# Optimization experiments

Measured on AMD Instinct MI355X. Metric: run time of the kernel, lower is better.

Reference implementation:

```python
import jax, jax.numpy as jnp
import numpy as np

B, S, D = 2, 2048, 1024
H, DH = 16, 64
DM = 4096
NEG = 1e10


def setup_inputs() -> dict:
    key = jax.random.key(0)
    ks = jax.random.split(key, 8)
    sc = 1.0 / np.sqrt(D)
    return {
        "x": jax.random.normal(ks[0], (B, S, D), jnp.float32),
        "W_Q": jax.random.normal(ks[1], (H, DH, D), jnp.float32) * sc,
        "W_K": jax.random.normal(ks[2], (H, DH, D), jnp.float32) * sc,
        "W_V": jax.random.normal(ks[3], (H, DH, D), jnp.float32) * sc,
        "W_O": jax.random.normal(ks[4], (D, H * DH), jnp.float32) * sc,
        "W_in": jax.random.normal(ks[5], (DM, D), jnp.float32) * sc,
        "b_in": jnp.zeros((DM,), jnp.float32),
        "W_out": jax.random.normal(ks[6], (D, DM), jnp.float32) * sc,
        "b_out": jnp.zeros((D,), jnp.float32),
    }


def reference(x, W_Q, W_K, W_V, W_O, W_in, b_in, W_out, b_out):
    b, s, d = x.shape
    d_head = W_Q.shape[1]
    # --- Attention (faithful to original einsum/mask formulation) ---
    q = jnp.einsum('ihd,bpd->biph', W_Q, x)
    k = jnp.einsum('ihd,bpd->biph', W_K, x)
    v = jnp.einsum('ihd,bpd->biph', W_V, x)
    scores = jnp.einsum('biph,biqh->biqp', k, q)  # [b,i,q,p]
    # original: t.tril(scores) - 1e10 * (1 - triu(ones)) ; mask buffer is triu
    triu = jnp.triu(jnp.ones((s, s), x.dtype))
    masked = jnp.tril(scores) - NEG * (1.0 - triu)
    attn = jax.nn.softmax(masked / np.sqrt(d_head), axis=-1)
    z = jnp.einsum('biph,biqp->biqh', v, attn)          # [b,i,q,h]
    z_flat = z.transpose(0, 2, 1, 3).reshape(b, s, -1)   # b q (i h)
    attn_out = jnp.einsum('df,bqf->bqd', W_O, z_flat)
    # --- Block residual structure (as written: x = attn(x); x = x + x) ---
    mid = attn_out + attn_out
    # --- MLP ---
    pre = jnp.einsum('md,bpd->bpm', W_in, mid) + b_in
    h = jax.nn.relu(pre)
    mlp_out = jnp.einsum('dm,bpm->bpd', W_out, h) + b_out
    return mid + mlp_out
```

## Files before the change

kernel.cpp:

```cpp
#include <hip/hip_runtime.h>
#include <hip/hip_bf16.h>
#include <stdint.h>

typedef unsigned short ushort_t;
typedef __attribute__((ext_vector_type(8))) short short8;
typedef __attribute__((ext_vector_type(4))) float floatx4;

#define DEV __device__ __forceinline__

DEV ushort_t f2b(float f) {
  uint32_t x = __float_as_uint(f);
  uint32_t r = (x + 0x7FFFu + ((x >> 16) & 1u)) >> 16;
  return (ushort_t)r;
}
DEV float b2f(ushort_t u) { return __uint_as_float(((uint32_t)u) << 16); }

DEV void async16(const ushort_t* g, ushort_t* l) {
  __builtin_amdgcn_global_load_lds(
      (const __attribute__((address_space(1))) void*)g,
      (__attribute__((address_space(3))) void*)l, 16, 0, 0);
}

struct Cvt7 {
  const float* src[7];
  ushort_t* dst[7];
  unsigned start[8];
};
__global__ void cvt_all(Cvt7 a) {
  unsigned idx = blockIdx.x * blockDim.x + threadIdx.x;
  if (idx >= a.start[7]) return;
  int seg = 0;
#pragma unroll
  for (int j = 1; j < 7; j++) seg += (idx >= a.start[j]) ? 1 : 0;
  unsigned off = idx - a.start[seg];
  float4 v = ((const float4*)a.src[seg])[off];
  ((ushort4*)a.dst[seg])[off] = make_ushort4(f2b(v.x), f2b(v.y), f2b(v.z), f2b(v.w));
}

template <int MODE, int MT>
__launch_bounds__(256)
__global__ void gemm_bt(const ushort_t* __restrict__ A, const ushort_t* __restrict__ Bm,
                        int M, int N, int K,
                        ushort_t* __restrict__ outB, float* __restrict__ outF,
                        const float* __restrict__ bias) {
  constexpr int TM = 32 * MT;
  __shared__ alignas(16) ushort_t As[TM * 64];
  __shared__ alignas(16) ushort_t Bs[128 * 64];
  const int tid = threadIdx.x;
  const int wave = tid >> 6, lane = tid & 63;
  const int wm = wave >> 1, wn = wave & 1;
  const int m0 = blockIdx.y * TM, n0 = blockIdx.x * 128;

  floatx4 acc[MT][4];
#pragma unroll
  for (int i = 0; i < MT; i++)
#pragma unroll
    for (int j = 0; j < 4; j++) acc[i][j] = (floatx4){0.f, 0.f, 0.f, 0.f};

  const int r8 = lane >> 3;
  const int scol = (((lane & 7) ^ (r8 & 7)) * 8);
  const ushort_t* gA = A + (size_t)(m0 + wave * (TM / 4) + r8) * K + scol;
  const ushort_t* gB = Bm + (size_t)(n0 + wave * 32 + r8) * K + scol;
  ushort_t* lA = As + wave * (TM / 4) * 64;
  ushort_t* lB = Bs + wave * 2048;

  const int fr = lane & 15, fq = lane >> 4;
  const int sw = fr & 7;
  const ushort_t* rdA = As + (wm * 16 * MT + fr) * 64;
  const ushort_t* rdB = Bs + (wn * 64 + fr) * 64;

  for (int k0 = 0; k0 < K; k0 += 64) {
#pragma unroll
    for (int j = 0; j < MT; j++) async16(gA + (size_t)j * 8 * K, lA + j * 512);
#pragma unroll
    for (int j = 0; j < 4; j++) async16(gB + (size_t)j * 8 * K, lB + j * 512);
    gA += 64; gB += 64;
    __syncthreads();
#pragma unroll
    for (int h = 0; h < 2; h++) {
      const int co = ((h * 4 + fq) ^ sw) * 8;
      short8 af[MT], bfv[4];
#pragma unroll
      for (int mt = 0; mt < MT; mt++) af[mt] = *(const short8*)(rdA + mt * 16 * 64 + co);
#pragma unroll
      for (int nt = 0; nt < 4; nt++) bfv[nt] = *(const short8*)(rdB + nt * 16 * 64 + co);
#pragma unroll
      for (int mt = 0; mt < MT; mt++)
#pragma unroll
        for (int nt = 0; nt < 4; nt++)
          acc[mt][nt] = __builtin_amdgcn_mfma_f32_16x16x32_bf16(af[mt], bfv[nt], acc[mt][nt], 0, 0, 0);
    }
    __syncthreads();
  }

  const int crow = m0 + wm * 16 * MT + (lane >> 4) * 4;
  const int ccol = n0 + wn * 64 + (lane & 15);
#pragma unroll
  for (int mt = 0; mt < MT; mt++)
#pragma unroll
    for (int nt = 0; nt < 4; nt++) {
      floatx4 a = acc[mt][nt];
#pragma unroll
      for (int r = 0; r < 4; r++) {
        const int gm = crow + mt * 16 + r;
        const int gn = ccol + nt * 16;
        const size_t idx = (size_t)gm * N + gn;
        float v = a[r];
        if constexpr (MODE == 0) {
          outB[idx] = f2b(v);
        } else if constexpr (MODE == 1) {
          float t = 2.f * v;
          outB[idx] = f2b(t);
          outF[idx] = t + bias[gn];
        } else if constexpr (MODE == 2) {
          float t = v + bias[gn];
          outB[idx] = f2b(t > 0.f ? t : 0.f);
        } else {
          outF[idx] += v;
        }
      }
    }
}

__launch_bounds__(256)
__global__ void attn1(const ushort_t* __restrict__ qkv,
                      float* __restrict__ eG, float* __restrict__ psumG) {
  const int c = blockIdx.x & 31;
  const int i = (blockIdx.x >> 5) & 15;
  const int b = blockIdx.x >> 9;
  const int t = threadIdx.x, wave = t >> 6, h = t & 63;
  const size_t rowbase = (size_t)b * 2048 * 3072;
  float vacc = 0.f;
#pragma unroll 4
  for (int r = 0; r < 16; r++) {
    const int s = c * 64 + wave * 16 + r;
    const size_t rb = rowbase + (size_t)s * 3072 + i * 64 + h;
    float q = b2f(qkv[rb]);
    float k = b2f(qkv[rb + 1024]);
    float v = b2f(qkv[rb + 2048]);
    float d = q * k;
#pragma unroll
    for (int off = 32; off > 0; off >>= 1) d += __shfl_xor(d, off, 64);
    if (h == 0) eG[((size_t)(b * 16 + i)) * 2048 + s] = __expf(d * 0.125f);
    vacc += v;
  }
  __shared__ float vs[4][64];
  vs[wave][h] = vacc;
  __syncthreads();
  if (t < 64)
    psumG[(((size_t)(b * 16 + i)) * 32 + c) * 64 + t] =
        vs[0][t] + vs[1][t] + vs[2][t] + vs[3][t];
}

__launch_bounds__(256)
__global__ void attn2(const ushort_t* __restrict__ qkv,
                      const float* __restrict__ eG, const float* __restrict__ psumG,
                      ushort_t* __restrict__ Z) {
  const int wave = threadIdx.x >> 6, h = threadIdx.x & 63;
  const int c = (blockIdx.x & 7) * 4 + wave;
  const int i = (blockIdx.x >> 3) & 15;
  const int b = blockIdx.x >> 7;
  const size_t rowbase = (size_t)b * 2048 * 3072;
  const size_t pbase = ((size_t)(b * 16 + i)) * 32;
  float run = 0.f;
#pragma unroll 8
  for (int cc = c + 1; cc < 32; cc++) run += psumG[(pbase + cc) * 64 + h];
  const size_t ebase = ((size_t)(b * 16 + i)) * 2048;
  for (int t4 = 3; t4 >= 0; t4--) {
    float vv[16], ee[16];
#pragma unroll
    for (int j = 0; j < 16; j++) {
      const int s = c * 64 + t4 * 16 + j;
      vv[j] = b2f(qkv[rowbase + (size_t)s * 3072 + 2048 + i * 64 + h]);
      ee[j] = eG[ebase + s];
    }
#pragma unroll
    for (int j = 15; j >= 0; j--) {
      const int s = c * 64 + t4 * 16 + j;
      float z = (ee[j] * vv[j] + run) / (ee[j] + (float)(2047 - s));
      Z[((size_t)b * 2048 + s) * 1024 + i * 64 + h] = f2b(z);
      run += vv[j];
    }
  }
}

extern "C" void kernel_launch(void* const* d_in, const int* in_sizes, int n_in,
                              void* d_out, int out_size, void* d_ws, size_t ws_size,
                              hipStream_t stream) {
  const float* x     = (const float*)d_in[0];
  const float* W_Q   = (const float*)d_in[1];
  const float* W_K   = (const float*)d_in[2];
  const float* W_V   = (const float*)d_in[3];
  const float* W_O   = (const float*)d_in[4];
  const float* W_in  = (const float*)d_in[5];
  const float* b_in  = (const float*)d_in[6];
  const float* W_out = (const float*)d_in[7];
  const float* b_out = (const float*)d_in[8];
  float* out = (float*)d_out;

  char* base = (char*)d_ws;
  const size_t MB = 1048576;
  ushort_t* Xb    = (ushort_t*)(base + 0 * MB);
  ushort_t* Wqkv  = (ushort_t*)(base + 8 * MB);
  ushort_t* WOb   = (ushort_t*)(base + 14 * MB);
  ushort_t* Z     = (ushort_t*)(base + 16 * MB);
  ushort_t* QKV   = (ushort_t*)(base + 24 * MB);
  ushort_t* midb  = (ushort_t*)(base + 48 * MB);
  ushort_t* Winb  = (ushort_t*)(base + 56 * MB);
  ushort_t* Woutb = (ushort_t*)(base + 64 * MB);
  ushort_t* Hb    = (ushort_t*)(base + 72 * MB);
  float*    eG    = (float*)(base + 104 * MB);
  float*    psumG = (float*)(base + 104 * MB + 262144);

  Cvt7 ca;
  ca.src[0] = x;     ca.dst[0] = Xb;
  ca.src[1] = W_Q;   ca.dst[1] = Wqkv;
  ca.src[2] = W_K;   ca.dst[2] = Wqkv + 1048576;
  ca.src[3] = W_V;   ca.dst[3] = Wqkv + 2097152;
  ca.src[4] = W_O;   ca.dst[4] = WOb;
  ca.src[5] = W_in;  ca.dst[5] = Winb;
  ca.src[6] = W_out; ca.dst[6] = Woutb;
  unsigned n4s[7] = {1048576, 262144, 262144, 262144, 262144, 1048576, 1048576};
  unsigned acc4 = 0;
  for (int j = 0; j < 7; j++) { ca.start[j] = acc4; acc4 += n4s[j]; }
  ca.start[7] = acc4;
  cvt_all<<<dim3((acc4 + 255) / 256), dim3(256), 0, stream>>>(ca);

  gemm_bt<0, 4><<<dim3(24, 32), 256, 0, stream>>>(Xb, Wqkv, 4096, 3072, 1024,
                                                  QKV, nullptr, nullptr);
  attn1<<<dim3(1024), 256, 0, stream>>>(QKV, eG, psumG);
  attn2<<<dim3(256), 256, 0, stream>>>(QKV, eG, psumG, Z);
  gemm_bt<1, 2><<<dim3(8, 64), 256, 0, stream>>>(Z, WOb, 4096, 1024, 1024,
                                                 midb, out, b_out);
  gemm_bt<2, 4><<<dim3(32, 32), 256, 0, stream>>>(midb, Winb, 4096, 4096, 1024,
                                                  Hb, nullptr, b_in);
  gemm_bt<3, 2><<<dim3(8, 64), 256, 0, stream>>>(Hb, Woutb, 4096, 1024, 4096,
                                                 nullptr, out, b_out);
}
```

Baseline: 300.6 us.

## Split-K the down-projection GEMM and swizzle block order for L2 reuse

The final MLP down-projection GEMM (K=4096) is split into two K halves across blockIdx.z. Each half writes fp32 partials to a workspace, and a new reduce kernel adds both partials into the output. This doubles the block count for that GEMM, which had only 512 blocks. Several GEMMs also get a grouped block-index swizzle (groups of 8 row tiles) to improve L2 reuse. The cost is extra partial-buffer traffic and one more kernel launch. The partial buffer reuses workspace regions that earlier stages no longer need.

Measured after the change: 292.2 us. 1.03x faster.

```diff
diff --git a/kernel.cpp b/kernel.cpp
--- a/kernel.cpp
+++ b/kernel.cpp
@@ -37,10 +37,10 @@
   ((ushort4*)a.dst[seg])[off] = make_ushort4(f2b(v.x), f2b(v.y), f2b(v.z), f2b(v.w));
 }
 
-template <int MODE, int MT>
+template <int MODE, int MT, bool SWZ>
 __launch_bounds__(256)
 __global__ void gemm_bt(const ushort_t* __restrict__ A, const ushort_t* __restrict__ Bm,
-                        int M, int N, int K,
+                        int M, int N, int Kd, int ldk,
                         ushort_t* __restrict__ outB, float* __restrict__ outF,
                         const float* __restrict__ bias) {
   constexpr int TM = 32 * MT;
@@ -49,7 +49,17 @@
   const int tid = threadIdx.x;
   const int wave = tid >> 6, lane = tid & 63;
   const int wm = wave >> 1, wn = wave & 1;
-  const int m0 = blockIdx.y * TM, n0 = blockIdx.x * 128;
+
+  int bx, by;
+  if constexpr (SWZ) {
+    const int f = blockIdx.x + gridDim.x * blockIdx.y;
+    by = (f & 7) + 8 * (f / (8 * gridDim.x));
+    bx = (f >> 3) % gridDim.x;
+  } else {
+    bx = blockIdx.x; by = blockIdx.y;
+  }
+  const int m0 = by * TM, n0 = bx * 128;
+  const int kz = blockIdx.z * Kd;
 
   floatx4 acc[MT][4];
 #pragma unroll
@@ -59,8 +69,8 @@
 
   const int r8 = lane >> 3;
   const int scol = (((lane & 7) ^ (r8 & 7)) * 8);
-  const ushort_t* gA = A + (size_t)(m0 + wave * (TM / 4) + r8) * K + scol;
-  const ushort_t* gB = Bm + (size_t)(n0 + wave * 32 + r8) * K + scol;
+  const ushort_t* gA = A + (size_t)(m0 + wave * (TM / 4) + r8) * ldk + kz + scol;
+  const ushort_t* gB = Bm + (size_t)(n0 + wave * 32 + r8) * ldk + kz + scol;
   ushort_t* lA = As + wave * (TM / 4) * 64;
   ushort_t* lB = Bs + wave * 2048;
 
@@ -69,11 +79,11 @@
   const ushort_t* rdA = As + (wm * 16 * MT + fr) * 64;
   const ushort_t* rdB = Bs + (wn * 64 + fr) * 64;
 
-  for (int k0 = 0; k0 < K; k0 += 64) {
-#pragma unroll
-    for (int j = 0; j < MT; j++) async16(gA + (size_t)j * 8 * K, lA + j * 512);
-#pragma unroll
-    for (int j = 0; j < 4; j++) async16(gB + (size_t)j * 8 * K, lB + j * 512);
+  for (int k0 = 0; k0 < Kd; k0 += 64) {
+#pragma unroll
+    for (int j = 0; j < MT; j++) async16(gA + (size_t)j * 8 * ldk, lA + j * 512);
+#pragma unroll
+    for (int j = 0; j < 4; j++) async16(gB + (size_t)j * 8 * ldk, lB + j * 512);
     gA += 64; gB += 64;
     __syncthreads();
 #pragma unroll
@@ -95,6 +105,7 @@
 
   const int crow = m0 + wm * 16 * MT + (lane >> 4) * 4;
   const int ccol = n0 + wn * 64 + (lane & 15);
+  const size_t zoff = (size_t)blockIdx.z * M * N;
 #pragma unroll
   for (int mt = 0; mt < MT; mt++)
 #pragma unroll
@@ -116,10 +127,25 @@
           float t = v + bias[gn];
           outB[idx] = f2b(t > 0.f ? t : 0.f);
         } else {
-          outF[idx] += v;
+          outF[zoff + idx] = v;
         }
       }
     }
+}
+
+__launch_bounds__(256)
+__global__ void reduce2(const float4* __restrict__ P, float4* __restrict__ out, int n4) {
+  int i = blockIdx.x * blockDim.x + threadIdx.x;
+  int st = gridDim.x * blockDim.x;
+  for (; i < n4; i += st) {
+    float4 a = out[i];
+    float4 p0 = P[i], p1 = P[i + 1048576];
+    a.x += p0.x + p1.x;
+    a.y += p0.y + p1.y;
+    a.z += p0.z + p1.z;
+    a.w += p0.w + p1.w;
+    out[i] = a;
+  }
 }
 
 __launch_bounds__(256)
@@ -209,6 +235,7 @@
   ushort_t* Winb  = (ushort_t*)(base + 56 * MB);
   ushort_t* Woutb = (ushort_t*)(base + 64 * MB);
   ushort_t* Hb    = (ushort_t*)(base + 72 * MB);
+  float*    P     = (float*)(base + 0 * MB);
   float*    eG    = (float*)(base + 104 * MB);
   float*    psumG = (float*)(base + 104 * MB + 262144);
 
@@ -226,14 +253,15 @@
   ca.start[7] = acc4;
   cvt_all<<<dim3((acc4 + 255) / 256), dim3(256), 0, stream>>>(ca);
 
-  gemm_bt<0, 4><<<dim3(24, 32), 256, 0, stream>>>(Xb, Wqkv, 4096, 3072, 1024,
-                                                  QKV, nullptr, nullptr);
+  gemm_bt<0, 4, true><<<dim3(24, 32), 256, 0, stream>>>(Xb, Wqkv, 4096, 3072, 1024, 1024,
+                                                        QKV, nullptr, nullptr);
   attn1<<<dim3(1024), 256, 0, stream>>>(QKV, eG, psumG);
   attn2<<<dim3(256), 256, 0, stream>>>(QKV, eG, psumG, Z);
-  gemm_bt<1, 2><<<dim3(8, 64), 256, 0, stream>>>(Z, WOb, 4096, 1024, 1024,
-                                                 midb, out, b_out);
-  gemm_bt<2, 4><<<dim3(32, 32), 256, 0, stream>>>(midb, Winb, 4096, 4096, 1024,
-                                                  Hb, nullptr, b_in);
-  gemm_bt<3, 2><<<dim3(8, 64), 256, 0, stream>>>(Hb, Woutb, 4096, 1024, 4096,
-                                                 nullptr, out, b_out);
-}
+  gemm_bt<1, 2, true><<<dim3(8, 64), 256, 0, stream>>>(Z, WOb, 4096, 1024, 1024, 1024,
+                                                       midb, out, b_out);
+  gemm_bt<2, 4, false><<<dim3(32, 32), 256, 0, stream>>>(midb, Winb, 4096, 4096, 1024, 1024,
+                                                         Hb, nullptr, b_in);
+  gemm_bt<3, 2, true><<<dim3(8, 64, 2), 256, 0, stream>>>(Hb, Woutb, 4096, 1024, 2048, 4096,
+                                                          nullptr, P, nullptr);
+  reduce2<<<dim3(1024), 256, 0, stream>>>((const float4*)P, (float4*)out, 1048576);
+}
```
